# Kernel tuning notes

Hardware: AMD Instinct MI355X
Metric: run time of the kernel (lower is better)

## Reference

```python
import jax, jax.numpy as jnp
import numpy as np

DIM = 256
HEADS = 4


def setup_inputs() -> dict:
    key = jax.random.key(0)
    k1, k2, k3, k4, k5 = jax.random.split(key, 5)
    x = jax.random.normal(k1, (8, DIM, 128, 128), dtype=jnp.float32)
    s_in = 1.0 / np.sqrt(DIM)
    Wqkv = jax.random.normal(k2, (DIM, 3 * DIM), dtype=jnp.float32) * s_in
    bqkv = jax.random.normal(k3, (3 * DIM,), dtype=jnp.float32) * 0.02
    Wproj = jax.random.normal(k4, (DIM, DIM), dtype=jnp.float32) * s_in
    bproj = jax.random.normal(k5, (DIM,), dtype=jnp.float32) * 0.02
    return {"x": x, "Wqkv": Wqkv, "bqkv": bqkv, "Wproj": Wproj, "bproj": bproj}


def reference(x, Wqkv, bqkv, Wproj, bproj):
    b, c, h, w = x.shape
    hd = c // HEADS  # head dim
    scale = hd ** -0.5
    # axis='h': (b c h w) -> (b*w, h, c)
    x_r = jnp.transpose(x, (0, 3, 2, 1)).reshape(b * w, h, c)
    qkv = x_r @ Wqkv + bqkv                              # [B, S, 3c]
    qkv = qkv.reshape(b * w, h, 3, HEADS, hd)
    qkv = jnp.transpose(qkv, (2, 0, 3, 1, 4))            # [3, B, H, S, d]
    q, k, v = qkv[0], qkv[1], qkv[2]
    attn = jax.nn.softmax(jnp.einsum('bhqd,bhkd->bhqk', q, k) * scale, axis=-1)
    out = jnp.einsum('bhqk,bhkd->bhqd', attn, v)         # [B, H, S, d]
    out = jnp.transpose(out, (0, 2, 1, 3)).reshape(b * w, h, c)
    out = out @ Wproj + bproj
    # (b*w, h, c) -> (b, c, h, w)
    out = out.reshape(b, w, h, c)
    return jnp.transpose(out, (0, 3, 2, 1))
```

## Files before the change

### kernel.cpp

```cpp
#include <hip/hip_runtime.h>


typedef _Float16 h4 __attribute__((ext_vector_type(4)));
typedef _Float16 h8 __attribute__((ext_vector_type(8)));
typedef float f4 __attribute__((ext_vector_type(4)));
typedef unsigned int u4 __attribute__((ext_vector_type(4)));

#define MFMA32(a, b, c) __builtin_amdgcn_mfma_f32_16x16x32_f16((a), (b), (c), 0, 0, 0)

__device__ __forceinline__ void gll16(const _Float16* g, _Float16* l) {
  __builtin_amdgcn_global_load_lds(
      (const __attribute__((address_space(1))) void*)g,
      (__attribute__((address_space(3))) void*)l, 16, 0, 0);
}

__global__ __launch_bounds__(256) void prep_w(const float* __restrict__ Wqkv,
                                              const float* __restrict__ Wproj,
                                              _Float16* __restrict__ wqt,
                                              _Float16* __restrict__ wpt) {
  int i = blockIdx.x * 256 + threadIdx.x;
  if (i < 768 * 256) {
    int f = i >> 8, c = i & 255;
    wqt[i] = (_Float16)Wqkv[c * 768 + f];
  } else {
    int j = i - 768 * 256;
    int f = j >> 8, c = j & 255;
    wpt[j] = (_Float16)Wproj[c * 256 + f];
  }
}

__global__ __launch_bounds__(256, 3) void k1f(const float* __restrict__ x,
                                              const _Float16* __restrict__ wqt,
                                              const float* __restrict__ bqkv,
                                              _Float16* __restrict__ qkv,
                                              int b_base, int nb) {
  const int wg = blockIdx.x;
  const int xcd = wg & 7, seq = wg >> 3;
  const int id = xcd * (nb * 32) + seq;
  const int hb = id & 127;
  const int rest = id >> 7;
  const int wh = rest & 1, bl = rest >> 1;
  const int b = b_base + bl;
  const int w0 = wh * 64;

  const int tid = threadIdx.x;
  const int lane = tid & 63, wv = tid >> 6;
  const int g = lane >> 4, l16 = lane & 15;
  const int wr = wv >> 1, wc = wv & 1;

  __shared__ __align__(16) char smem[51200];
  _Float16* sXT = (_Float16*)smem;
  _Float16* sA = (_Float16*)(smem + 33792);
  _Float16* sO = (_Float16*)(smem + 33792);

  {
    const int j0 = tid & 7, r8 = tid >> 3;
#pragma unroll
    for (int p = 0; p < 8; ++p) {
      const int c = p * 32 + r8;
      const float* src = x + (((long)b * 256 + c) * 128 + hb) * 128 + w0;
      f4 v0 = *(const f4*)(src + j0 * 4);
      f4 v1 = *(const f4*)(src + (j0 + 8) * 4);
#pragma unroll
      for (int i = 0; i < 4; ++i) {
        sXT[(j0 * 4 + i) * 264 + c] = (_Float16)v0[i];
        sXT[((j0 + 8) * 4 + i) * 264 + c] = (_Float16)v1[i];
      }
    }
  }
  __syncthreads();

  const int r0 = wv * 32;
  const int rl = lane >> 3;
  const int chs = ((lane & 7) ^ rl) * 8;
  const int wl = tid >> 2, dc = tid & 3;
  const int kx = (l16 & 7) * 8;
  const int tB = wc * 32 + l16;

  for (int ft = 0; ft < 6; ++ft) {
    const int f0 = ft * 128;
    f4 acc[4][2];
#pragma unroll
    for (int mt = 0; mt < 4; ++mt)
#pragma unroll
      for (int nt = 0; nt < 2; ++nt)
#pragma unroll
        for (int r = 0; r < 4; ++r) acc[mt][nt][r] = 0.f;

    for (int kc = 0; kc < 4; ++kc) {
      h8 bfr[2][2];
#pragma unroll
      for (int ks = 0; ks < 2; ++ks)
#pragma unroll
        for (int nt = 0; nt < 2; ++nt)
          bfr[ks][nt] = *(const h8*)(sXT + (tB + nt * 16) * 264 + kc * 64 +
                                     ks * 32 + 8 * g);
#pragma unroll
      for (int i = 0; i < 4; ++i) {
        const int row = r0 + i * 8 + rl;
        gll16(wqt + (long)(f0 + row) * 256 + kc * 64 + chs, sA + (r0 + i * 8) * 64);
      }
      __syncthreads();
#pragma unroll
      for (int ks = 0; ks < 2; ++ks) {
        const int kk = (ks * 32 + 8 * g) ^ kx;
        h8 af[4];
#pragma unroll
        for (int mt = 0; mt < 4; ++mt)
          af[mt] = *(const h8*)(sA + (wr * 64 + mt * 16 + l16) * 64 + kk);
#pragma unroll
        for (int mt = 0; mt < 4; ++mt)
#pragma unroll
          for (int nt = 0; nt < 2; ++nt)
            acc[mt][nt] = MFMA32(af[mt], bfr[ks][nt], acc[mt][nt]);
      }
      __syncthreads();
    }

#pragma unroll
    for (int mt = 0; mt < 4; ++mt) {
      f4 bb = *(const f4*)(bqkv + f0 + wr * 64 + mt * 16 + 4 * g);
#pragma unroll
      for (int nt = 0; nt < 2; ++nt) {
        const int tl = wc * 32 + nt * 16 + l16;
#pragma unroll
        for (int r = 0; r < 4; ++r)
          sO[tl * 136 + wr * 64 + mt * 16 + 4 * g + r] =
              (_Float16)(acc[mt][nt][r] + bb[r]);
      }
    }
    __syncthreads();
#pragma unroll
    for (int h2 = 0; h2 < 2; ++h2) {
      const int fh = f0 + h2 * 64;
      const int qi = fh >> 8, head = (fh >> 6) & 3;
      _Float16* dst = qkv + (((long)(qi * nb + bl) * 4 + head) * 128 + hb) * 8192 +
                      (w0 + wl) * 64 + dc * 16;
      const _Float16* s = sO + wl * 136 + h2 * 64 + dc * 16;
      *(u4*)dst = *(const u4*)s;
      *(u4*)(dst + 8) = *(const u4*)(s + 8);
    }
    __syncthreads();
  }
}

__global__ __launch_bounds__(256) void k2_attn(const _Float16* __restrict__ qkv,
                                               _Float16* __restrict__ attnout,
                                               int nb) {
  const int w = blockIdx.x, head = blockIdx.y, bl = blockIdx.z;
  const int tid = threadIdx.x;
  const int lane = tid & 63, wv = tid >> 6;
  const int g = lane >> 4, l16 = lane & 15;

  __shared__ __align__(16) char smem[(128 * 72 * 2 + 64 * 136) * 2];
  _Float16* sQ = (_Float16*)smem;
  _Float16* sK = sQ + 128 * 72;
  _Float16* sVT = sK + 128 * 72;
  _Float16* sP = sQ;
  _Float16* sO = sQ;

  const long base = (((long)bl * 4 + head) * 128) * 8192 + (long)w * 64;
  const long QS = (long)nb * 4 * 128 * 8192;
  const _Float16* qg = qkv + base;
  const _Float16* kg = qkv + base + QS;
  const _Float16* vg = qkv + base + 2 * QS;

#pragma unroll
  for (int i = 0; i < 4; ++i) {
    int u = tid + 256 * i;
    int hh = u >> 3, dq = u & 7;
    *(u4*)(sQ + hh * 72 + dq * 8) = *(const u4*)(qg + (long)hh * 8192 + dq * 8);
    *(u4*)(sK + hh * 72 + dq * 8) = *(const u4*)(kg + (long)hh * 8192 + dq * 8);
  }
  {
    const int hh = tid & 127, dcv = tid >> 7;
#pragma unroll
    for (int jj = 0; jj < 4; ++jj) {
      u4 vv = *(const u4*)(vg + (long)hh * 8192 + dcv * 32 + jj * 8);
      const _Float16* pe = (const _Float16*)&vv;
#pragma unroll
      for (int e = 0; e < 8; ++e)
        sVT[(dcv * 32 + jj * 8 + e) * 136 + hh] = pe[e];
    }
  }
  __syncthreads();

  f4 accS[8][2];
  for (int i = 0; i < 8; ++i)
    for (int jt = 0; jt < 2; ++jt)
      for (int r = 0; r < 4; ++r) accS[i][jt][r] = 0.f;
#pragma unroll
  for (int ks = 0; ks < 2; ++ks) {
    const int k = ks * 32 + 8 * g;
    h8 af[8], bf[2];
#pragma unroll
    for (int i = 0; i < 8; ++i)
      af[i] = *(const h8*)(sK + (i * 16 + l16) * 72 + k);
#pragma unroll
    for (int jt = 0; jt < 2; ++jt)
      bf[jt] = *(const h8*)(sQ + (wv * 32 + jt * 16 + l16) * 72 + k);
#pragma unroll
    for (int i = 0; i < 8; ++i)
#pragma unroll
      for (int jt = 0; jt < 2; ++jt)
        accS[i][jt] = MFMA32(af[i], bf[jt], accS[i][jt]);
  }

  float rinv[2];
#pragma unroll
  for (int jt = 0; jt < 2; ++jt) {
    float m = -1e30f;
    for (int i = 0; i < 8; ++i)
      for (int r = 0; r < 4; ++r) m = fmaxf(m, accS[i][jt][r]);
    m = fmaxf(m, __shfl_xor(m, 16));
    m = fmaxf(m, __shfl_xor(m, 32));
    float s = 0.f;
    for (int i = 0; i < 8; ++i)
      for (int r = 0; r < 4; ++r) {
        float p = __expf((accS[i][jt][r] - m) * 0.125f);
        accS[i][jt][r] = p;
        s += p;
      }
    s += __shfl_xor(s, 16);
    s += __shfl_xor(s, 32);
    rinv[jt] = 1.0f / s;
  }

  __syncthreads();
#pragma unroll
  for (int jt = 0; jt < 2; ++jt) {
    const int hq = wv * 32 + jt * 16 + l16;
#pragma unroll
    for (int i = 0; i < 8; ++i) {
      h4 pv;
      pv[0] = (_Float16)accS[i][jt][0];
      pv[1] = (_Float16)accS[i][jt][1];
      pv[2] = (_Float16)accS[i][jt][2];
      pv[3] = (_Float16)accS[i][jt][3];
      *(h4*)(sP + hq * 136 + i * 16 + 4 * g) = pv;
    }
  }
  __syncthreads();

  f4 accO[4][2];
  for (int mt = 0; mt < 4; ++mt)
    for (int jt = 0; jt < 2; ++jt)
      for (int r = 0; r < 4; ++r) accO[mt][jt][r] = 0.f;
#pragma unroll
  for (int i2 = 0; i2 < 4; ++i2) {
    const int k = i2 * 32 + 8 * g;
    h8 av[4], pb[2];
#pragma unroll
    for (int mt = 0; mt < 4; ++mt)
      av[mt] = *(const h8*)(sVT + (mt * 16 + l16) * 136 + k);
#pragma unroll
    for (int jt = 0; jt < 2; ++jt)
      pb[jt] = *(const h8*)(sP + (wv * 32 + jt * 16 + l16) * 136 + k);
#pragma unroll
    for (int mt = 0; mt < 4; ++mt)
#pragma unroll
      for (int jt = 0; jt < 2; ++jt)
        accO[mt][jt] = MFMA32(av[mt], pb[jt], accO[mt][jt]);
  }

  __syncthreads();
#pragma unroll
  for (int mt = 0; mt < 4; ++mt)
#pragma unroll
    for (int jt = 0; jt < 2; ++jt)
#pragma unroll
      for (int r = 0; r < 4; ++r)
        sO[(wv * 32 + jt * 16 + l16) * 72 + mt * 16 + 4 * g + r] =
            (_Float16)(accO[mt][jt][r] * rinv[jt]);
  __syncthreads();

  const int hh = tid >> 1, d0 = (tid & 1) * 32;
  const _Float16* s = sO + hh * 72 + d0;
  _Float16* dst = attnout + ((long)bl * 16384 + hh * 128 + w) * 256 + head * 64 + d0;
#pragma unroll
  for (int e = 0; e < 4; ++e)
    *(u4*)(dst + e * 8) = *(const u4*)(s + e * 8);
}

__global__ __launch_bounds__(256, 4) void k3_proj(const _Float16* __restrict__ attnout,
                                                  const _Float16* __restrict__ wpt,
                                                  const float* __restrict__ bproj,
                                                  float* __restrict__ out,
                                                  int b_base, int nb) {
  const int ct = blockIdx.x, tt = blockIdx.y, bl = blockIdx.z;
  const int b = b_base + bl;
  const int tid = threadIdx.x;
  const int lane = tid & 63, wv = tid >> 6;
  const int g = lane >> 4, l16 = lane & 15;
  const int wr = wv >> 1, wc = wv & 1;
  const int co0 = ct * 128;
  const long t0 = (long)tt * 128;

  __shared__ __align__(16) char smem[33792];
  _Float16* sA = (_Float16*)smem;
  _Float16* sB = sA + 128 * 64;
  float* sOut = (float*)smem;

  f4 acc[4][4];
#pragma unroll
  for (int mt = 0; mt < 4; ++mt)
#pragma unroll
    for (int nt = 0; nt < 4; ++nt)
#pragma unroll
      for (int r = 0; r < 4; ++r) acc[mt][nt][r] = 0.f;

  const _Float16* Ab = wpt + (long)co0 * 256;
  const _Float16* Bb = attnout + ((long)bl * 16384 + t0) * 256;
  const int r0 = wv * 32;
  const int rl = lane >> 3;
  const int chs = ((lane & 7) ^ rl) * 8;
  const int kx = (l16 & 7) * 8;

  for (int kc = 0; kc < 4; ++kc) {
    const int c0 = kc * 64;
#pragma unroll
    for (int i = 0; i < 4; ++i) {
      const int row = r0 + i * 8 + rl;
      gll16(Ab + (long)row * 256 + c0 + chs, sA + (r0 + i * 8) * 64);
      gll16(Bb + (long)row * 256 + c0 + chs, sB + (r0 + i * 8) * 64);
    }
    __syncthreads();
#pragma unroll
    for (int ks = 0; ks < 2; ++ks) {
      const int kk = (ks * 32 + 8 * g) ^ kx;
      h8 af[4], bf[4];
#pragma unroll
      for (int mt = 0; mt < 4; ++mt)
        af[mt] = *(const h8*)(sA + (wr * 64 + mt * 16 + l16) * 64 + kk);
#pragma unroll
      for (int nt = 0; nt < 4; ++nt)
        bf[nt] = *(const h8*)(sB + (wc * 64 + nt * 16 + l16) * 64 + kk);
#pragma unroll
      for (int mt = 0; mt < 4; ++mt)
#pragma unroll
        for (int nt = 0; nt < 4; ++nt)
          acc[mt][nt] = MFMA32(af[mt], bf[nt], acc[mt][nt]);
    }
    __syncthreads();
  }

#pragma unroll
  for (int h2 = 0; h2 < 2; ++h2) {
    if (h2) __syncthreads();
    if (wr == h2) {
#pragma unroll
      for (int mt = 0; mt < 4; ++mt) {
        f4 bb = *(const f4*)(bproj + co0 + h2 * 64 + mt * 16 + 4 * g);
#pragma unroll
        for (int nt = 0; nt < 4; ++nt)
#pragma unroll
          for (int r = 0; r < 4; ++r)
            sOut[(mt * 16 + 4 * g + r) * 132 + wc * 64 + nt * 16 + l16] =
                acc[mt][nt][r] + bb[r];
      }
    }
    __syncthreads();
    const int row = tid >> 2, seg = (tid & 3) * 32;
    const float* s = sOut + row * 132 + seg;
    float* dst = out + ((long)b * 256 + co0 + h2 * 64 + row) * 16384 + t0 + seg;
#pragma unroll
    for (int e = 0; e < 8; ++e)
      *(f4*)(dst + e * 4) = *(const f4*)(s + e * 4);
  }
}

extern "C" void kernel_launch(void* const* d_in, const int* in_sizes, int n_in,
                              void* d_out, int out_size, void* d_ws, size_t ws_size,
                              hipStream_t stream) {
  const float* x = (const float*)d_in[0];
  const float* Wqkv = (const float*)d_in[1];
  const float* bqkv = (const float*)d_in[2];
  const float* Wproj = (const float*)d_in[3];
  const float* bproj = (const float*)d_in[4];
  float* out = (float*)d_out;

  char* ws = (char*)d_ws;
  const long WQT = 393216L, WPT = 131072L;
  const long PER_B = 25165824L + 8388608L;
  long nb_l = ((long)ws_size - (WQT + WPT)) / PER_B;
  int nb = nb_l < 1 ? 1 : (nb_l > 8 ? 8 : (int)nb_l);

  _Float16* wqt = (_Float16*)ws;
  _Float16* wpt = (_Float16*)(ws + WQT);
  _Float16* qkv = (_Float16*)(ws + WQT + WPT);
  _Float16* attnout = (_Float16*)(ws + WQT + WPT + (long)nb * 25165824L);

  prep_w<<<1024, 256, 0, stream>>>(Wqkv, Wproj, wqt, wpt);

  for (int b0 = 0; b0 < 8; b0 += nb) {
    int nbv = (8 - b0 < nb) ? (8 - b0) : nb;
    k1f<<<nbv * 256, 256, 0, stream>>>(x, wqt, bqkv, qkv, b0, nbv);
    k2_attn<<<dim3(128, 4, nbv), 256, 0, stream>>>(qkv, attnout, nbv);
    k3_proj<<<dim3(2, 128, nbv), 256, 0, stream>>>(attnout, wpt, bproj, out, b0, nbv);
  }
}
```

Baseline: 242.5 us.

## Pre-swizzle Wqkv into MFMA fragment order and load A directly from global

The weight-prep kernel now writes Wqkv in a fragment-major layout that matches the per-lane MFMA A-operand order. The QKV projection kernel then loads each lane's A fragment straight from global memory (L2-resident) instead of staging it through LDS with global_load_lds. This drops the per-k-chunk LDS staging and both __syncthreads barriers in the inner loop. In exchange, every wave re-reads weights from global or L2 with full-latency loads and no LDS sharing, so performance now depends on cache hit rates and on latency hiding.

```diff
diff --git a/kernel.cpp b/kernel.cpp
--- a/kernel.cpp
+++ b/kernel.cpp
@@ -16,21 +16,24 @@
 
 __global__ __launch_bounds__(256) void prep_w(const float* __restrict__ Wqkv,
                                               const float* __restrict__ Wproj,
-                                              _Float16* __restrict__ wqt,
+                                              _Float16* __restrict__ wqtf,
                                               _Float16* __restrict__ wpt) {
   int i = blockIdx.x * 256 + threadIdx.x;
   if (i < 768 * 256) {
     int f = i >> 8, c = i & 255;
-    wqt[i] = (_Float16)Wqkv[c * 768 + f];
+    int ft = f >> 7, wr = (f >> 6) & 1, mt = (f >> 4) & 3, l16 = f & 15;
+    int kc = c >> 6, ks = (c >> 5) & 1, gg = (c >> 3) & 3, j = c & 7;
+    int frag = (ft * 2 + wr) * 32 + mt * 8 + kc * 2 + ks;
+    wqtf[(long)frag * 512 + (gg * 16 + l16) * 8 + j] = (_Float16)Wqkv[c * 768 + f];
   } else {
-    int j = i - 768 * 256;
-    int f = j >> 8, c = j & 255;
-    wpt[j] = (_Float16)Wproj[c * 256 + f];
+    int jj = i - 768 * 256;
+    int f = jj >> 8, c = jj & 255;
+    wpt[jj] = (_Float16)Wproj[c * 256 + f];
   }
 }
 
 __global__ __launch_bounds__(256, 3) void k1f(const float* __restrict__ x,
-                                              const _Float16* __restrict__ wqt,
+                                              const _Float16* __restrict__ wqtf,
                                               const float* __restrict__ bqkv,
                                               _Float16* __restrict__ qkv,
                                               int b_base, int nb) {
@@ -50,7 +53,6 @@
 
   __shared__ __align__(16) char smem[51200];
   _Float16* sXT = (_Float16*)smem;
-  _Float16* sA = (_Float16*)(smem + 33792);
   _Float16* sO = (_Float16*)(smem + 33792);
 
   {
@@ -70,11 +72,7 @@
   }
   __syncthreads();
 
-  const int r0 = wv * 32;
-  const int rl = lane >> 3;
-  const int chs = ((lane & 7) ^ rl) * 8;
   const int wl = tid >> 2, dc = tid & 3;
-  const int kx = (l16 & 7) * 8;
   const int tB = wc * 32 + l16;
 
   for (int ft = 0; ft < 6; ++ft) {
@@ -87,6 +85,8 @@
 #pragma unroll
         for (int r = 0; r < 4; ++r) acc[mt][nt][r] = 0.f;
 
+    const _Float16* Af = wqtf + (long)(ft * 2 + wr) * 32 * 512 + lane * 8;
+#pragma unroll
     for (int kc = 0; kc < 4; ++kc) {
       h8 bfr[2][2];
 #pragma unroll
@@ -96,25 +96,17 @@
           bfr[ks][nt] = *(const h8*)(sXT + (tB + nt * 16) * 264 + kc * 64 +
                                      ks * 32 + 8 * g);
 #pragma unroll
-      for (int i = 0; i < 4; ++i) {
-        const int row = r0 + i * 8 + rl;
-        gll16(wqt + (long)(f0 + row) * 256 + kc * 64 + chs, sA + (r0 + i * 8) * 64);
-      }
-      __syncthreads();
-#pragma unroll
       for (int ks = 0; ks < 2; ++ks) {
-        const int kk = (ks * 32 + 8 * g) ^ kx;
         h8 af[4];
 #pragma unroll
         for (int mt = 0; mt < 4; ++mt)
-          af[mt] = *(const h8*)(sA + (wr * 64 + mt * 16 + l16) * 64 + kk);
+          af[mt] = *(const h8*)(Af + (mt * 8 + kc * 2 + ks) * 512);
 #pragma unroll
         for (int mt = 0; mt < 4; ++mt)
 #pragma unroll
           for (int nt = 0; nt < 2; ++nt)
             acc[mt][nt] = MFMA32(af[mt], bfr[ks][nt], acc[mt][nt]);
       }
-      __syncthreads();
     }
 
 #pragma unroll
@@ -385,16 +377,16 @@
   long nb_l = ((long)ws_size - (WQT + WPT)) / PER_B;
   int nb = nb_l < 1 ? 1 : (nb_l > 8 ? 8 : (int)nb_l);
 
-  _Float16* wqt = (_Float16*)ws;
+  _Float16* wqtf = (_Float16*)ws;
   _Float16* wpt = (_Float16*)(ws + WQT);
   _Float16* qkv = (_Float16*)(ws + WQT + WPT);
   _Float16* attnout = (_Float16*)(ws + WQT + WPT + (long)nb * 25165824L);
 
-  prep_w<<<1024, 256, 0, stream>>>(Wqkv, Wproj, wqt, wpt);
+  prep_w<<<1024, 256, 0, stream>>>(Wqkv, Wproj, wqtf, wpt);
 
   for (int b0 = 0; b0 < 8; b0 += nb) {
     int nbv = (8 - b0 < nb) ? (8 - b0) : nb;
-    k1f<<<nbv * 256, 256, 0, stream>>>(x, wqt, bqkv, qkv, b0, nbv);
+    k1f<<<nbv * 256, 256, 0, stream>>>(x, wqtf, bqkv, qkv, b0, nbv);
     k2_attn<<<dim3(128, 4, nbv), 256, 0, stream>>>(qkv, attnout, nbv);
     k3_proj<<<dim3(2, 128, nbv), 256, 0, stream>>>(attnout, wpt, bproj, out, b0, nbv);
   }
```

Measured after the change: 254.7 us. 5.0% more time.
